# Performance work log

Measured on AMD Instinct MI355X. Metric: run time of the kernel, lower is better.

Reference implementation:

```python
import jax, jax.numpy as jnp
import numpy as np

N = 16384; C = 16; H = 256; W = 704
HEADS = 4; PTS = 4; K = 8; DH = C // HEADS
EPS = 1e-3  # BatchNorm eps from module

def _bn(x, g, b):
    # BatchNorm1d in training mode: batch statistics over N
    mu = x.mean(axis=0)
    var = x.var(axis=0)
    return (x - mu) * jax.lax.rsqrt(var + EPS) * g + b

def setup_inputs():
    key = jax.random.key(0)
    ks = jax.random.split(key, 20)
    def w(i, shape, s=0.25):
        return jax.random.normal(ks[i], shape, jnp.float32) * s
    grid_y = jax.random.randint(ks[0], (N,), 0, H)
    grid_x = jax.random.randint(ks[1], (N,), 0, W)
    return {
        "point_features": jax.random.normal(ks[2], (N, C), jnp.float32),
        "image_feat": jax.random.normal(ks[3], (C, H, W), jnp.float32),
        "image_grid": jnp.stack([grid_y, grid_x], axis=1),
        "Wk": w(4, (C, C)), "bk": w(5, (C,)), "gk": jnp.ones((C,)), "betak": jnp.zeros((C,)),
        "Wfc": w(6, (2, C)), "bfc": w(7, (C,)), "gfc": jnp.ones((C,)), "betafc": jnp.zeros((C,)),
        "Wt": w(8, (C, C)), "bt": w(9, (C,)), "gt": jnp.ones((C,)), "betat": jnp.zeros((C,)),
        "Woff": w(10, (C, HEADS * PTS * 2), 0.02), "boff": w(11, (HEADS * PTS * 2,), 0.5),
        "Wattn": w(12, (C, HEADS * PTS), 0.02), "battn": jnp.zeros((HEADS * PTS,)),
        "Wval": w(13, (C, C)), "bval": w(14, (C,)),
        "Wout": w(15, (C, C)), "bout": w(16, (C,)),
        "Wf": w(17, (2 * C, C)), "bf": w(18, (C,)), "gf": jnp.ones((C,)), "betaf": jnp.zeros((C,)),
    }

def _deform_attn(q, image_feat, grid_f, Woff, boff, Wattn, battn, Wval, bval, Wout, bout):
    # MSDeformAttn with 1 level: learned offsets around projected pixel, bilinear sampling
    n = q.shape[0]
    off = (q @ Woff + boff).reshape(n, HEADS, PTS, 2)
    attn = jax.nn.softmax((q @ Wattn + battn).reshape(n, HEADS, PTS), axis=-1)
    val = (image_feat.reshape(C, H * W).T @ Wval + bval).reshape(H * W, HEADS, DH)
    val_h = val.transpose(1, 0, 2)  # [HEADS, HW, DH]
    loc_y = grid_f[:, 0][:, None, None] + off[..., 0]  # [N, HEADS, PTS]
    loc_x = grid_f[:, 1][:, None, None] + off[..., 1]
    y0 = jnp.floor(loc_y); x0 = jnp.floor(loc_x)
    wy = loc_y - y0; wx = loc_x - x0

    def corner(yi, xi, wgt):
        valid = (yi >= 0) & (yi <= H - 1) & (xi >= 0) & (xi <= W - 1)
        yc = jnp.clip(yi, 0, H - 1).astype(jnp.int32)
        xc = jnp.clip(xi, 0, W - 1).astype(jnp.int32)
        idx = (yc * W + xc).transpose(1, 0, 2)  # [HEADS, N, PTS]
        g = jax.vmap(lambda v, i: v[i])(val_h, idx)  # [HEADS, N, PTS, DH]
        return g * (wgt * valid).transpose(1, 0, 2)[..., None]

    samp = (corner(y0, x0, (1 - wy) * (1 - wx))
            + corner(y0, x0 + 1, (1 - wy) * wx)
            + corner(y0 + 1, x0, wy * (1 - wx))
            + corner(y0 + 1, x0 + 1, wy * wx))  # [HEADS, N, PTS, DH]
    out = (samp * attn.transpose(1, 0, 2)[..., None]).sum(axis=2)  # [HEADS, N, DH]
    out = out.transpose(1, 0, 2).reshape(n, C)
    return out @ Wout + bout

def reference(point_features, image_feat, image_grid, Wk, bk, gk, betak, Wfc, bfc, gfc, betafc, Wt, bt, gt, betat, Woff, boff, Wattn, battn, Wval, bval, Wout, bout, Wf, bf, gf, betaf):
    grid_f = image_grid.astype(jnp.float32)
    # KNN over projected pixel coords (cKDTree.query k=K+1, drop self)
    d2 = ((grid_f[:, None, :] - grid_f[None, :, :]) ** 2).sum(-1)
    _, nidx = jax.lax.top_k(-d2, K + 1)
    nidx = nidx[:, 1:]  # [N, K]

    pts = _bn(point_features @ Wk + bk, gk, betak)  # pts_key_proj
    # normalized relative image-plane positions -> fc
    center = grid_f.mean(axis=0)
    rel = grid_f - center
    mx = jnp.abs(rel).max(axis=0)
    mx = jnp.where(mx == 0, 1.0, mx)
    pos = _bn((rel / mx) @ Wfc + bfc, gfc, betafc)

    # gather image feats at projected pixels + KNN-graph neighbor aggregation
    gathered = image_feat[:, image_grid[:, 0], image_grid[:, 1]].T  # [N, C]
    neigh = gathered[nidx].mean(axis=1)  # [N, C]

    q = pts + pos
    img_pre = _deform_attn(q, image_feat, grid_f, Woff, boff, Wattn, battn, Wval, bval, Wout, bout) + neigh

    pts_pre = _bn(pts @ Wt + bt, gt, betat)  # pts_transform
    fuse = jax.nn.relu(jnp.concatenate([pts_pre, img_pre], axis=-1))  # activate_out
    return jax.nn.relu(_bn(fuse @ Wf + bf, gf, betaf))  # fuse_conv
```

## Files before the change

kernel.cpp:

```cpp
#include <hip/hip_runtime.h>
#include <climits>

#define N_ 16384
#define C_ 16
#define H_ 256
#define W_ 704
#define HW_ (H_*W_)
#define NC_ (N_*C_)
#define EPS_ 1e-3f
#define HDR_ 512

typedef unsigned long long ull;

#define FLIN_  (HDR_ + 8*NC_)
#define VAL_   (HDR_ + 9*NC_)
#define KNNI_  (VAL_ + HW_*16)
#define PARTF_ (KNNI_ + 378256)
#define PS_    (PARTF_ + 16384)
#define GP_    (PS_ + 17408)
#define IMFT_  (GP_ + 640)

#define CAP_ 6144
#define PPB_ 32

#define LOAD16(dst, src) { const float4* _s=(const float4*)(src); float4 _a=_s[0],_b=_s[1],_c=_s[2],_d=_s[3]; \
  dst[0]=_a.x;dst[1]=_a.y;dst[2]=_a.z;dst[3]=_a.w; dst[4]=_b.x;dst[5]=_b.y;dst[6]=_b.z;dst[7]=_b.w; \
  dst[8]=_c.x;dst[9]=_c.y;dst[10]=_c.z;dst[11]=_c.w; dst[12]=_d.x;dst[13]=_d.y;dst[14]=_d.z;dst[15]=_d.w; }

#define STORE16(dst, src) { float4* _d=(float4*)(dst); \
  _d[0]=make_float4(src[0],src[1],src[2],src[3]); _d[1]=make_float4(src[4],src[5],src[6],src[7]); \
  _d[2]=make_float4(src[8],src[9],src[10],src[11]); _d[3]=make_float4(src[12],src[13],src[14],src[15]); }

__global__ __launch_bounds__(256) void k_init(float* ws){
  if (blockIdx.x < 176){
    int4* c = (int4*)(ws + KNNI_);
    c[blockIdx.x*256 + threadIdx.x] = make_int4(0,0,0,0);
  } else if (threadIdx.x == 0){
    int* ih = (int*)ws;
    ih[2]=INT_MAX; ih[3]=INT_MIN; ih[4]=INT_MAX; ih[5]=INT_MIN;
  }
}

__global__ __launch_bounds__(256) void k_statsprep(
    const float* __restrict__ pf, const float* __restrict__ imf,
    const int* __restrict__ grid,
    const float* __restrict__ Wval, const float* __restrict__ bval,
    float* __restrict__ ws)
{
  int t = threadIdx.x;
  if (blockIdx.x < 64){
    __shared__ float sP[4096];
    __shared__ double sDP[20];
    __shared__ int sh[16];
    int i = blockIdx.x*256 + t;
    { const float4* s4=(const float4*)(pf+i*16);
      float4* d4=(float4*)(sP+t*16);
      d4[0]=s4[0]; d4[1]=s4[1]; d4[2]=s4[2]; d4[3]=s4[3]; }
    int2 g = ((const int2*)grid)[i];
    int* counts = (int*)(ws + KNNI_);
    atomicAdd(&counts[g.x*W_ + g.y], 1);
    int mny=g.x,mxy=g.x,mnx=g.y,mxx=g.y;
#pragma unroll
    for (int o=32;o>0;o>>=1){
      mny=min(mny,__shfl_down(mny,o)); mxy=max(mxy,__shfl_down(mxy,o));
      mnx=min(mnx,__shfl_down(mnx,o)); mxx=max(mxx,__shfl_down(mxx,o));
    }
    int wv = t>>6;
    if ((t&63)==0){ sh[wv]=mny; sh[4+wv]=mxy; sh[8+wv]=mnx; sh[12+wv]=mxx; }
    double yy=(double)g.x, xx=(double)g.y;
    double m0=yy,m1=xx,m2=yy*yy,m3=xx*xx,m4=yy*xx;
#pragma unroll
    for (int o=32;o>0;o>>=1){
      m0+=__shfl_down(m0,o); m1+=__shfl_down(m1,o); m2+=__shfl_down(m2,o);
      m3+=__shfl_down(m3,o); m4+=__shfl_down(m4,o);
    }
    if ((t&63)==0){ sDP[wv*5]=m0; sDP[wv*5+1]=m1; sDP[wv*5+2]=m2; sDP[wv*5+3]=m3; sDP[wv*5+4]=m4; }
    __syncthreads();
    if (t==0){
      int* ih=(int*)ws;
      atomicMin(&ih[2],min(min(sh[0],sh[1]),min(sh[2],sh[3])));
      atomicMax(&ih[3],max(max(sh[4],sh[5]),max(sh[6],sh[7])));
      atomicMin(&ih[4],min(min(sh[8],sh[9]),min(sh[10],sh[11])));
      atomicMax(&ih[5],max(max(sh[12],sh[13]),max(sh[14],sh[15])));
      double* GP=(double*)(ws+GP_)+blockIdx.x*5;
#pragma unroll
      for (int k=0;k<5;++k) GP[k]=sDP[k]+sDP[5+k]+sDP[10+k]+sDP[15+k];
    }
    float* PS = ws + PS_ + blockIdx.x*272;
    int a=t&15, b2=t>>4;
    float acc=0.f;
    for (int i2=0;i2<256;++i2) acc += sP[i2*16+a]*sP[i2*16+b2];
    PS[16+t]=acc;
    if (t<16){
      float s=0.f;
      for (int i2=0;i2<256;++i2) s += sP[i2*16+t];
      PS[t]=s;
    }
  } else {
    __shared__ float sW[256], sb[16];
    sW[t]=Wval[t];
    if (t<16) sb[t]=bval[t];
    __syncthreads();
    int pix=(blockIdx.x-64)*256+t;
    float a[16];
#pragma unroll
    for (int ci=0;ci<16;++ci) a[ci]=imf[ci*HW_+pix];
    STORE16(ws+IMFT_+pix*16, a);
    float o[16];
#pragma unroll
    for (int c=0;c<16;++c) o[c]=sb[c];
#pragma unroll
    for (int ci=0;ci<16;++ci){ float v=a[ci];
#pragma unroll
      for (int c=0;c<16;++c) o[c]+=v*sW[ci*16+c];
    }
    STORE16(ws+VAL_+pix*16, o);
  }
}

__global__ __launch_bounds__(256) void k_scanA(float* ws){
  const int* counts = (const int*)(ws + KNNI_);
  int* bsum = (int*)(ws + KNNI_) + 180224 + 180240;
  int t = threadIdx.x;
  int v = counts[blockIdx.x*256 + t];
#pragma unroll
  for (int o=32;o>0;o>>=1) v += __shfl_down(v,o);
  __shared__ int w4[4];
  if ((t&63)==0) w4[t>>6] = v;
  __syncthreads();
  if (t==0) bsum[blockIdx.x] = w4[0]+w4[1]+w4[2]+w4[3];
}

__global__ __launch_bounds__(256) void k_scanB(
    const float* __restrict__ Wk, const float* __restrict__ bk,
    const float* __restrict__ gk, const float* __restrict__ betak,
    const float* __restrict__ Wfc, const float* __restrict__ bfc,
    const float* __restrict__ gfc, const float* __restrict__ betafc,
    const float* __restrict__ Wt, const float* __restrict__ bt,
    const float* __restrict__ gt, const float* __restrict__ betat,
    float* __restrict__ ws)
{
  __shared__ float sS[256], sSum[16];
  __shared__ float skA[16], skC[16];
  __shared__ double sG[5];
  __shared__ float sCtr[4];
  int t = threadIdx.x;
  const float* PS = ws + PS_;
  float acc=0.f, acc2=0.f;
  for (int b=0;b<64;++b){
    acc += PS[b*272 + t];
    if (t<16) acc2 += PS[b*272 + 256 + t];
  }
  if (t<16){ sSum[t]=acc; sS[240+t]=acc2; }
  else sS[t-16]=acc;
  if (t<5){
    const double* GP=(const double*)(ws+GP_);
    double s=0.0;
    for (int b=0;b<64;++b) s += GP[b*5+t];
    sG[t]=s;
  }
  __syncthreads();
  if (t==0){
    const int* ih=(const int*)ws;
    float cy=(float)(sG[0]/(double)N_), cx=(float)(sG[1]/(double)N_);
    float my=fmaxf((float)ih[3]-cy, cy-(float)ih[2]);
    float mx=fmaxf((float)ih[5]-cx, cx-(float)ih[4]);
    if (my==0.f) my=1.f;
    if (mx==0.f) mx=1.f;
    sCtr[0]=cy; sCtr[1]=cx; sCtr[2]=1.f/my; sCtr[3]=1.f/mx;
    ws[264]=cy; ws[265]=cx; ws[266]=sCtr[2]; ws[267]=sCtr[3];
  }
  __syncthreads();
  const float invN = 1.f/(float)N_;
  if (t<16){
    float wc[16];
#pragma unroll
    for (int j=0;j<16;++j) wc[j]=Wk[j*16+t];
    float dotS=0.f;
#pragma unroll
    for (int a2=0;a2<16;++a2) dotS+=sSum[a2]*wc[a2];
    float qd=0.f;
#pragma unroll
    for (int b2=0;b2<16;++b2){
      float inner=0.f;
#pragma unroll
      for (int a2=0;a2<16;++a2) inner+=wc[a2]*sS[b2*16+a2];
      qd+=wc[b2]*inner;
    }
    float bkc=bk[t];
    float mu = dotS*invN + bkc;
    float ex2 = qd*invN + 2.f*bkc*dotS*invN + bkc*bkc;
    float var = ex2 - mu*mu;
    float a = gk[t]/sqrtf(var+EPS_);
    skA[t]=a; skC[t]=betak[t]-mu*a;
    ws[136+t]=a; ws[152+t]=skC[t];
    float cy=sCtr[0], cx=sCtr[1], imy=sCtr[2], imx=sCtr[3];
    float Eyy=((float)(sG[2]/(double)N_) - cy*cy)*imy*imy;
    float Exx=((float)(sG[3]/(double)N_) - cx*cx)*imx*imx;
    float Eyx=((float)(sG[4]/(double)N_) - cy*cx)*imy*imx;
    float W0=Wfc[t], W1=Wfc[16+t];
    float varfc = Eyy*W0*W0 + 2.f*Eyx*W0*W1 + Exx*W1*W1;
    float afc = gfc[t]/sqrtf(varfc+EPS_);
    ws[168+t]=afc; ws[184+t]=betafc[t]-bfc[t]*afc;
  }
  __syncthreads();
  if (t<16){
    float Ac[16];
#pragma unroll
    for (int j=0;j<16;++j){
      float s=0.f;
#pragma unroll
      for (int m=0;m<16;++m) s += Wk[j*16+m]*skA[m]*Wt[m*16+t];
      Ac[j]=s;
    }
    float dc=bt[t];
#pragma unroll
    for (int m=0;m<16;++m) dc += (bk[m]*skA[m]+skC[m])*Wt[m*16+t];
    float dotS=0.f;
#pragma unroll
    for (int a2=0;a2<16;++a2) dotS+=sSum[a2]*Ac[a2];
    float qd=0.f;
#pragma unroll
    for (int b2=0;b2<16;++b2){
      float inner=0.f;
#pragma unroll
      for (int a2=0;a2<16;++a2) inner+=Ac[a2]*sS[b2*16+a2];
      qd+=Ac[b2]*inner;
    }
    float mu = dotS*invN + dc;
    float ex2 = qd*invN + 2.f*dc*dotS*invN + dc*dc;
    float var = ex2 - mu*mu;
    float a = gt[t]/sqrtf(var+EPS_);
    ws[200+t]=a; ws[216+t]=betat[t]-mu*a;
  }
  __syncthreads();
  int* bsum = (int*)(ws + KNNI_) + 180224 + 180240;
  int* boff = bsum + 704;
  __shared__ int sWsum[4];
  __shared__ int sCarry;
  int lane=t&63, wv=t>>6;
  if (t==0) sCarry=0;
  __syncthreads();
  for (int c=0;c<3;++c){
    int idx=c*256+t;
    int v0=(idx<704)?bsum[idx]:0;
    int v=v0;
#pragma unroll
    for (int o=1;o<64;o<<=1){ int xx=__shfl_up(v,o); if (lane>=o) v+=xx; }
    if (lane==63) sWsum[wv]=v;
    __syncthreads();
    int add=sCarry;
    for (int w2=0;w2<wv;++w2) add+=sWsum[w2];
    if (idx<704) boff[idx]=add+v-v0;
    __syncthreads();
    if (t==255) sCarry=add+v;
    __syncthreads();
  }
}

__global__ __launch_bounds__(256) void k_scanC(float* ws){
  int* counts = (int*)(ws + KNNI_);
  int* cellst = counts + 180224;
  const int* boff = counts + 180224 + 180240 + 704;
  __shared__ int sWsum[4];
  int t=threadIdx.x, lane=t&63, wv=t>>6;
  int i=blockIdx.x*256+t;
  int v0=counts[i], v=v0;
#pragma unroll
  for (int o=1;o<64;o<<=1){ int xx=__shfl_up(v,o); if (lane>=o) v+=xx; }
  if (lane==63) sWsum[wv]=v;
  __syncthreads();
  int add=boff[blockIdx.x];
  for (int w2=0;w2<wv;++w2) add+=sWsum[w2];
  int start=add+v-v0;
  cellst[i]=start;
  counts[i]=start;
  if (i==0) cellst[HW_]=N_;
}

__global__ __launch_bounds__(256) void k_scatter(const int* __restrict__ grid, float* __restrict__ ws){
  int i=blockIdx.x*256+threadIdx.x;
  int2 g=((const int2*)grid)[i];
  int* counts=(int*)(ws+KNNI_);
  unsigned* psort=(unsigned*)(counts+180224+180240+704+704);
  int pos=atomicAdd(&counts[g.x*W_+g.y],1);
  psort[pos]=((unsigned)g.x<<24)|((unsigned)g.y<<14)|(unsigned)i;
}

__device__ __forceinline__ void knn_insert(ull* arr, ull key){
  if (key < arr[8]){
    int q=8;
    while (q>0 && arr[q-1]>key){ arr[q]=arr[q-1]; --q; }
    arr[q]=key;
  }
}

__device__ __forceinline__ void scan_rows_global(const int* __restrict__ cellst,
                                                 const unsigned* __restrict__ psort,
                                                 int y, int x, int s,
                                                 int y0, int y1, int x0, int x1, ull* arr){
  for (int yy=y0+s; yy<=y1; yy+=4){
    int rowb=yy*W_;
    int st=cellst[rowb+x0];
    int e =cellst[rowb+x1+1];
    int dy=y-yy, dy2=dy*dy;
    for (int p=st;p<e;++p){
      unsigned u=psort[p];
      int px=(int)((u>>14)&1023);
      int dx=x-px;
      knn_insert(arr, ((ull)(unsigned)(dy2+dx*dx)<<14)|(ull)(u&16383u));
    }
  }
}

__device__ __forceinline__ void scan_rows_band(const unsigned* sBand, const int* sRowBase,
                                               int ya, int y, int x, int s,
                                               int y0, int y1, int x0, int x1, ull* arr){
  for (int yy=y0+s; yy<=y1; yy+=4){
    int j=yy-ya;
    int b=sRowBase[j], e=sRowBase[j+1];
    int lo=b, hi=e;
    while (lo<hi){ int mid=(lo+hi)>>1; int xm=(int)((sBand[mid]>>14)&1023); if (xm<x0) lo=mid+1; else hi=mid; }
    int dy=y-yy, dy2=dy*dy;
    for (int p=lo;p<e;++p){
      unsigned u=sBand[p];
      int px=(int)((u>>14)&1023);
      if (px>x1) break;
      int dx=x-px;
      knn_insert(arr, ((ull)(unsigned)(dy2+dx*dx)<<14)|(ull)(u&16383u));
    }
  }
}

__global__ __launch_bounds__(128) void k_mega(
    const float* __restrict__ pf, const int* __restrict__ grid,
    const float* __restrict__ Wk, const float* __restrict__ bk,
    const float* __restrict__ Wfc, const float* __restrict__ bfc,
    const float* __restrict__ Wt, const float* __restrict__ bt,
    const float* __restrict__ Woff, const float* __restrict__ boff,
    const float* __restrict__ Wattn, const float* __restrict__ battn,
    const float* __restrict__ Wout, const float* __restrict__ bout,
    const float* __restrict__ Wf, const float* __restrict__ bf,
    float* __restrict__ ws)
{
  __shared__ float sWk[256], sWt[256], sWattn[256], sWout[256];
  __shared__ float sWoff[512], sWf[512], sWfc[32];
  __shared__ float sbk[16], sbfc[16], sbt[16], sboff[32], sbattn[16], sbout[16], sbf[16];
  __shared__ float skA[16], skC[16], sfcA[16], sfcC[16], stA[16], stC[16];
  __shared__ float sCtr[4];
  __shared__ unsigned sMe[PPB_];
  __shared__ int sMn, sMx;
  __shared__ unsigned sBand[CAP_];
  __shared__ int sRowBase[80];
  __shared__ float sTl[512], sNei[512], sOf[1024], sAt[512], sSamp[512], sImg[512];
  __shared__ float sPart[64];

  const int* cellst = (const int*)(ws+KNNI_)+180224;
  const unsigned* psort = (const unsigned*)((const int*)(ws+KNNI_)+180224+180240+704+704);
  int tid=threadIdx.x, lane=tid&63;
  for (int j=tid;j<256;j+=128){ sWk[j]=Wk[j]; sWt[j]=Wt[j]; sWattn[j]=Wattn[j]; sWout[j]=Wout[j]; }
  for (int j=tid;j<512;j+=128){ sWoff[j]=Woff[j]; sWf[j]=Wf[j]; }
  if (tid<32){ sWfc[tid]=Wfc[tid]; sboff[tid]=boff[tid]; }
  if (tid<16){
    sbk[tid]=bk[tid]; sbfc[tid]=bfc[tid]; sbt[tid]=bt[tid]; sbattn[tid]=battn[tid];
    sbout[tid]=bout[tid]; sbf[tid]=bf[tid];
    skA[tid]=ws[136+tid]; skC[tid]=ws[152+tid];
    sfcA[tid]=ws[168+tid]; sfcC[tid]=ws[184+tid];
    stA[tid]=ws[200+tid]; stC[tid]=ws[216+tid];
  }
  if (tid<4) sCtr[tid]=ws[264+tid];
  if (tid==0){ sMn=INT_MAX; sMx=-1; }
  if (tid<PPB_) sMe[tid]=psort[blockIdx.x*PPB_+tid];
  __syncthreads();
  if (tid<PPB_){
    int yy=(int)(sMe[tid]>>24);
    atomicMin(&sMn,yy); atomicMax(&sMx,yy);
  }
  __syncthreads();
  int ya=max(sMn-16,0), yb=min(sMx+16,H_-1);
  int nr=yb-ya+1;
  int p0=cellst[ya*W_], p1=cellst[(yb+1)*W_];
  int count=p1-p0;
  bool fb=(count>CAP_)||(nr>78);
  if (tid<PPB_){
    unsigned me=sMe[tid];
    int i=(int)(me&16383u);
    float yf=(float)(me>>24), xf=(float)((me>>14)&1023u);
    float p[16]; LOAD16(p, pf+i*16);
    float ok[16];
#pragma unroll
    for (int c=0;c<16;++c) ok[c]=sbk[c];
#pragma unroll
    for (int j=0;j<16;++j){ float v=p[j];
#pragma unroll
      for (int c=0;c<16;++c) ok[c]+=v*sWk[j*16+c];
    }
    float ry=(yf-sCtr[0])*sCtr[2], rx=(xf-sCtr[1])*sCtr[3];
    float pts[16], q[16];
#pragma unroll
    for (int c=0;c<16;++c){
      pts[c]=ok[c]*skA[c]+skC[c];
      float pos=ry*sWfc[c]+rx*sWfc[16+c]+sbfc[c];
      q[c]=pts[c]+pos*sfcA[c]+sfcC[c];
    }
    float tv[16];
#pragma unroll
    for (int c=0;c<16;++c) tv[c]=sbt[c];
#pragma unroll
    for (int j=0;j<16;++j){ float v=pts[j];
#pragma unroll
      for (int c=0;c<16;++c) tv[c]+=v*sWt[j*16+c];
    }
#pragma unroll
    for (int c=0;c<16;++c) sTl[tid*16+c]=fmaxf(tv[c]*stA[c]+stC[c],0.f);
    float ov[32];
#pragma unroll
    for (int o=0;o<32;++o) ov[o]=sboff[o];
#pragma unroll
    for (int j=0;j<16;++j){ float v=q[j];
#pragma unroll
      for (int o=0;o<32;++o) ov[o]+=v*sWoff[j*32+o];
    }
#pragma unroll
    for (int o=0;o<32;++o) sOf[tid*32+o]=ov[o];
    float l[16];
#pragma unroll
    for (int c=0;c<16;++c) l[c]=sbattn[c];
#pragma unroll
    for (int j=0;j<16;++j){ float v=q[j];
#pragma unroll
      for (int c=0;c<16;++c) l[c]+=v*sWattn[j*16+c];
    }
#pragma unroll
    for (int h=0;h<4;++h){
      float m=fmaxf(fmaxf(l[h*4],l[h*4+1]),fmaxf(l[h*4+2],l[h*4+3]));
      float e0=expf(l[h*4]-m),e1=expf(l[h*4+1]-m),e2=expf(l[h*4+2]-m),e3=expf(l[h*4+3]-m);
      float inv=1.f/(e0+e1+e2+e3);
      sAt[tid*16+h*4]=e0*inv; sAt[tid*16+h*4+1]=e1*inv;
      sAt[tid*16+h*4+2]=e2*inv; sAt[tid*16+h*4+3]=e3*inv;
    }
  } else {
    int tt=tid-PPB_;
    if (!fb){
      for (int j=tt;j<count;j+=96) sBand[j]=psort[p0+j];
      for (int j=tt;j<=nr;j+=96) sRowBase[j]=cellst[(ya+j)*W_]-p0;
    }
  }
  __syncthreads();
  int s=tid&3, pl=tid>>2;
  unsigned meK=sMe[pl];
  int y=(int)(meK>>24), x=(int)((meK>>14)&1023u);
  int r=8;
  { int y0=max(y-8,0),y1=min(y+8,H_-1),x0=max(x-8,0),x1=min(x+8,W_-1);
    if ((y1-y0+1)*(x1-x0+1)<224) r=16; }
  ull arr[9];
#pragma unroll
  for (int q2=0;q2<9;++q2) arr[q2]=~0ull;
  {
    int y0=max(y-r,0),y1=min(y+r,H_-1),x0=max(x-r,0),x1=min(x+r,W_-1);
    if (!fb) scan_rows_band(sBand,sRowBase,ya,y,x,s,y0,y1,x0,x1,arr);
    else     scan_rows_global(cellst,psort,y,x,s,y0,y1,x0,x1,arr);
  }
  ull m[9];
  bool done=false;
  {
    ull k[9];
#pragma unroll
    for (int q2=0;q2<9;++q2) m[q2]=~0ull;
    int base=lane&~3;
    for (int ss=0;ss<4;++ss){
#pragma unroll
      for (int q2=0;q2<9;++q2) k[q2]=__shfl(arr[q2],base+ss);
      for (int q3=0;q3<9;++q3){
        ull kk=k[q3];
        if (kk>=m[8]) break;
        int q=8; while (q>0&&m[q-1]>kk){ m[q]=m[q-1]; --q; } m[q]=kk;
      }
    }
    int y0=max(y-r,0),y1=min(y+r,H_-1),x0=max(x-r,0),x1=min(x+r,W_-1);
    bool covered=(y0==0)&&(y1==H_-1)&&(x0==0)&&(x1==W_-1);
    bool ok2=covered;
    if (!ok2 && m[8]!=~0ull){ int d9=(int)(m[8]>>14); ok2 = d9 < (r+1)*(r+1); }
    done=ok2;
  }
  while (__ballot(!done)){
    if (!done){
      r<<=1;
      int y0=max(y-r,0),y1=min(y+r,H_-1),x0=max(x-r,0),x1=min(x+r,W_-1);
#pragma unroll
      for (int q2=0;q2<9;++q2) arr[q2]=~0ull;
      if (!fb && r<=16) scan_rows_band(sBand,sRowBase,ya,y,x,s,y0,y1,x0,x1,arr);
      else              scan_rows_global(cellst,psort,y,x,s,y0,y1,x0,x1,arr);
    }
    ull k[9];
    bool doIns=!done;
    if (doIns){
#pragma unroll
      for (int q2=0;q2<9;++q2) m[q2]=~0ull;
    }
    int base=lane&~3;
    for (int ss=0;ss<4;++ss){
#pragma unroll
      for (int q2=0;q2<9;++q2) k[q2]=__shfl(arr[q2],base+ss);
      if (doIns){
        for (int q3=0;q3<9;++q3){
          ull kk=k[q3];
          if (kk>=m[8]) break;
          int q=8; while (q>0&&m[q-1]>kk){ m[q]=m[q-1]; --q; } m[q]=kk;
        }
      }
    }
    if (!done){
      int y0=max(y-r,0),y1=min(y+r,H_-1),x0=max(x-r,0),x1=min(x+r,W_-1);
      bool covered=(y0==0)&&(y1==H_-1)&&(x0==0)&&(x1==W_-1);
      bool ok2=covered;
      if (!ok2 && m[8]!=~0ull){ int d9=(int)(m[8]>>14); ok2 = d9 < (r+1)*(r+1); }
      if (ok2) done=true;
    }
  }
  {
    const float* imfT = ws + IMFT_;
    int pixn[8];
#pragma unroll
    for (int nb=0;nb<8;++nb){
      int idx=(int)(m[nb+1]&16383ull);
      int2 g2=((const int2*)grid)[idx];
      pixn[nb]=g2.x*W_+g2.y;
    }
    float4 v[8];
#pragma unroll
    for (int nb=0;nb<8;++nb) v[nb]=*(const float4*)(imfT+pixn[nb]*16+s*4);
    float4 acc=make_float4(0.f,0.f,0.f,0.f);
#pragma unroll
    for (int nb=0;nb<8;++nb){
      acc.x+=v[nb].x; acc.y+=v[nb].y; acc.z+=v[nb].z; acc.w+=v[nb].w;
    }
    ((float4*)sNei)[tid]=make_float4(acc.x*0.125f,acc.y*0.125f,acc.z*0.125f,acc.w*0.125f);
  }
  __syncthreads();
  {
    int p=tid>>2, h=tid&3;
    unsigned meA=sMe[p];
    float yf=(float)(meA>>24), xf=(float)((meA>>14)&1023u);
    const float4* val4=(const float4*)(ws+VAL_);
    int addr[16];
    float wgt[16];
#pragma unroll
    for (int pt=0;pt<4;++pt){
      float a=sAt[p*16+h*4+pt];
      float ly=yf+sOf[p*32+h*8+pt*2], lx=xf+sOf[p*32+h*8+pt*2+1];
      float fy=floorf(ly), fx=floorf(lx);
      float wy=ly-fy, wx=lx-fx;
      int y0=(int)fy, x0=(int)fx;
#pragma unroll
      for (int k2=0;k2<4;++k2){
        int yy=y0+(k2>>1), xx=x0+(k2&1);
        bool valid=((unsigned)yy<(unsigned)H_)&&((unsigned)xx<(unsigned)W_);
        int yc=min(max(yy,0),H_-1), xc=min(max(xx,0),W_-1);
        addr[pt*4+k2]=(yc*W_+xc)*4+h;
        float ww=((k2>>1)?wy:(1.f-wy))*((k2&1)?wx:(1.f-wx));
        wgt[pt*4+k2]=valid?a*ww:0.f;
      }
    }
    float4 acc=make_float4(0.f,0.f,0.f,0.f);
#pragma unroll
    for (int b2=0;b2<2;++b2){
      float4 vv[8];
#pragma unroll
      for (int k2=0;k2<8;++k2) vv[k2]=val4[addr[b2*8+k2]];
#pragma unroll
      for (int k2=0;k2<8;++k2){
        float w2=wgt[b2*8+k2];
        acc.x+=w2*vv[k2].x; acc.y+=w2*vv[k2].y; acc.z+=w2*vv[k2].z; acc.w+=w2*vv[k2].w;
      }
    }
    ((float4*)sSamp)[tid]=acc;
    __syncthreads();
    float img[4];
#pragma unroll
    for (int k2=0;k2<4;++k2){ int cc=h*4+k2; img[k2]=sbout[cc]+sNei[p*16+cc]; }
#pragma unroll
    for (int j=0;j<16;++j){
      float v=sSamp[p*16+j];
#pragma unroll
      for (int k2=0;k2<4;++k2) img[k2]+=v*sWout[j*16+h*4+k2];
    }
    ((float4*)sImg)[tid]=make_float4(img[0],img[1],img[2],img[3]);
    __syncthreads();
    float fl[4];
#pragma unroll
    for (int k2=0;k2<4;++k2) fl[k2]=sbf[h*4+k2];
#pragma unroll
    for (int j=0;j<16;++j){
      float v1=sTl[p*16+j];
      float v2=fmaxf(sImg[p*16+j],0.f);
#pragma unroll
      for (int k2=0;k2<4;++k2){
        fl[k2]+=v1*sWf[j*16+h*4+k2];
        fl[k2]+=v2*sWf[(16+j)*16+h*4+k2];
      }
    }
    int i3=(int)(meA&16383u);
    ((float4*)(ws+FLIN_+i3*16))[h]=make_float4(fl[0],fl[1],fl[2],fl[3]);
    float s0=fl[0],s1=fl[1],s2=fl[2],s3=fl[3];
    float q0=fl[0]*fl[0],q1=fl[1]*fl[1],q2=fl[2]*fl[2],q3=fl[3]*fl[3];
#pragma unroll
    for (int o=32;o>=4;o>>=1){
      s0+=__shfl_down(s0,o); s1+=__shfl_down(s1,o); s2+=__shfl_down(s2,o); s3+=__shfl_down(s3,o);
      q0+=__shfl_down(q0,o); q1+=__shfl_down(q1,o); q2+=__shfl_down(q2,o); q3+=__shfl_down(q3,o);
    }
    int wave=tid>>6, lane2=tid&63;
    if (lane2<4){
      sPart[wave*32+lane2*4+0]=s0; sPart[wave*32+lane2*4+1]=s1;
      sPart[wave*32+lane2*4+2]=s2; sPart[wave*32+lane2*4+3]=s3;
      sPart[wave*32+16+lane2*4+0]=q0; sPart[wave*32+16+lane2*4+1]=q1;
      sPart[wave*32+16+lane2*4+2]=q2; sPart[wave*32+16+lane2*4+3]=q3;
    }
    __syncthreads();
    if (tid<32){
      float v=sPart[tid]+sPart[32+tid];
      (ws+PARTF_)[blockIdx.x*32+tid]=v;
    }
  }
}

__global__ __launch_bounds__(256) void k_outf(const float* __restrict__ gf,
                                              const float* __restrict__ betaf,
                                              const float* __restrict__ ws,
                                              float* __restrict__ out){
  __shared__ float red[256];
  __shared__ float sA[16], sC[16];
  int t=threadIdx.x, slot=t&31, chunk=t>>5;
  const float* part=ws+PARTF_;
  float acc=0.f;
  for (int bb=chunk*64; bb<chunk*64+64; ++bb) acc+=part[bb*32+slot];
  red[t]=acc;
  __syncthreads();
  if (chunk==0){
    float v=red[slot];
#pragma unroll
    for (int k2=1;k2<8;++k2) v+=red[k2*32+slot];
    red[slot]=v;
  }
  __syncthreads();
  if (t<16){
    float mu=red[t]*(1.f/N_);
    float var=red[16+t]*(1.f/N_)-mu*mu;
    float a=gf[t]/sqrtf(var+EPS_);
    sA[t]=a; sC[t]=betaf[t]-mu*a;
  }
  __syncthreads();
  int base=blockIdx.x*4096+t*16;
  float fl[16]; LOAD16(fl, ws+FLIN_+base);
  float o[16];
#pragma unroll
  for (int c=0;c<16;++c) o[c]=fmaxf(fl[c]*sA[c]+sC[c],0.f);
  STORE16(out+base, o);
}

extern "C" void kernel_launch(void* const* d_in, const int* in_sizes, int n_in,
                              void* d_out, int out_size, void* d_ws, size_t ws_size,
                              hipStream_t stream)
{
  const float* pf    = (const float*)d_in[0];
  const float* imf   = (const float*)d_in[1];
  const int*   gridp = (const int*)d_in[2];
  const float* Wk   =(const float*)d_in[3],  *bk   =(const float*)d_in[4];
  const float* gk   =(const float*)d_in[5],  *betak=(const float*)d_in[6];
  const float* Wfc  =(const float*)d_in[7],  *bfc  =(const float*)d_in[8];
  const float* gfc  =(const float*)d_in[9],  *betafc=(const float*)d_in[10];
  const float* Wt   =(const float*)d_in[11], *bt   =(const float*)d_in[12];
  const float* gt   =(const float*)d_in[13], *betat=(const float*)d_in[14];
  const float* Woff =(const float*)d_in[15], *boff =(const float*)d_in[16];
  const float* Wattn=(const float*)d_in[17], *battn=(const float*)d_in[18];
  const float* Wval =(const float*)d_in[19], *bval =(const float*)d_in[20];
  const float* Wout =(const float*)d_in[21], *bout =(const float*)d_in[22];
  const float* Wf   =(const float*)d_in[23], *bf   =(const float*)d_in[24];
  const float* gf   =(const float*)d_in[25], *betaf=(const float*)d_in[26];
  float* ws  = (float*)d_ws;
  float* out = (float*)d_out;

  hipLaunchKernelGGL(k_init,      dim3(177),     dim3(256), 0, stream, ws);
  hipLaunchKernelGGL(k_statsprep, dim3(768),     dim3(256), 0, stream, pf, imf, gridp, Wval, bval, ws);
  hipLaunchKernelGGL(k_scanA,     dim3(704),     dim3(256), 0, stream, ws);
  hipLaunchKernelGGL(k_scanB,     dim3(1),       dim3(256), 0, stream,
                     Wk, bk, gk, betak, Wfc, bfc, gfc, betafc, Wt, bt, gt, betat, ws);
  hipLaunchKernelGGL(k_scanC,     dim3(704),     dim3(256), 0, stream, ws);
  hipLaunchKernelGGL(k_scatter,   dim3(N_/256),  dim3(256), 0, stream, gridp, ws);
  hipLaunchKernelGGL(k_mega,      dim3(N_/PPB_), dim3(128), 0, stream,
                     pf, gridp, Wk, bk, Wfc, bfc, Wt, bt, Woff, boff, Wattn, battn,
                     Wout, bout, Wf, bf, ws);
  hipLaunchKernelGGL(k_outf,      dim3(64),      dim3(256), 0, stream, gf, betaf, ws, out);
}
```

Measured before the change: 234.8 us.

## Prefetch deformable samples before KNN, pack coords in keys, shrink shared memory

Moves the bilinear-sample address computation and the 16 value gathers for deformable attention ahead of the KNN search, so those global loads are in flight while the KNN scan runs. KNN keys now store the distance in the high 32 bits plus index and pixel coordinates, which removes the extra grid lookup per neighbour. sSamp and sImg now reuse the sBand buffer, and the band capacity shrinks, cutting LDS use so more blocks can be resident. The costs are 16 float4 values held in registers across the KNN phase, which can raise register pressure, and a global-read fallback more often when a band does not fit the smaller buffer. The key ordering also changes, so ties in distance now break by index first and then by coordinates.

Result: no change. 236.0 us (+0.5%).

```diff
diff --git a/kernel.cpp b/kernel.cpp
--- a/kernel.cpp
+++ b/kernel.cpp
@@ -20,7 +20,7 @@
 #define GP_    (PS_ + 17408)
 #define IMFT_  (GP_ + 640)
 
-#define CAP_ 6144
+#define CAP_ 3584
 #define PPB_ 32
 
 #define LOAD16(dst, src) { const float4* _s=(const float4*)(src); float4 _a=_s[0],_b=_s[1],_c=_s[2],_d=_s[3]; \
@@ -287,6 +287,11 @@
   psort[pos]=((unsigned)g.x<<24)|((unsigned)g.y<<14)|(unsigned)i;
 }
 
+__device__ __forceinline__ ull make_key(int d2, unsigned u){
+  return ((ull)(unsigned)d2<<32) | ((ull)(u&16383u)<<18) |
+         ((ull)(u>>24)<<10) | (ull)((u>>14)&1023u);
+}
+
 __device__ __forceinline__ void knn_insert(ull* arr, ull key){
   if (key < arr[8]){
     int q=8;
@@ -308,7 +313,7 @@
       unsigned u=psort[p];
       int px=(int)((u>>14)&1023);
       int dx=x-px;
-      knn_insert(arr, ((ull)(unsigned)(dy2+dx*dx)<<14)|(ull)(u&16383u));
+      knn_insert(arr, make_key(dy2+dx*dx, u));
     }
   }
 }
@@ -327,13 +332,13 @@
       int px=(int)((u>>14)&1023);
       if (px>x1) break;
       int dx=x-px;
-      knn_insert(arr, ((ull)(unsigned)(dy2+dx*dx)<<14)|(ull)(u&16383u));
+      knn_insert(arr, make_key(dy2+dx*dx, u));
     }
   }
 }
 
 __global__ __launch_bounds__(128) void k_mega(
-    const float* __restrict__ pf, const int* __restrict__ grid,
+    const float* __restrict__ pf,
     const float* __restrict__ Wk, const float* __restrict__ bk,
     const float* __restrict__ Wfc, const float* __restrict__ bfc,
     const float* __restrict__ Wt, const float* __restrict__ bt,
@@ -352,8 +357,10 @@
   __shared__ int sMn, sMx;
   __shared__ unsigned sBand[CAP_];
   __shared__ int sRowBase[80];
-  __shared__ float sTl[512], sNei[512], sOf[1024], sAt[512], sSamp[512], sImg[512];
+  __shared__ float sTl[512], sNei[512], sOf[1024], sAt[512];
   __shared__ float sPart[64];
+  float* sSamp = (float*)sBand;
+  float* sImg  = ((float*)sBand) + 512;
 
   const int* cellst = (const int*)(ws+KNNI_)+180224;
   const unsigned* psort = (const unsigned*)((const int*)(ws+KNNI_)+180224+180240+704+704);
@@ -448,6 +455,33 @@
   }
   __syncthreads();
   int s=tid&3, pl=tid>>2;
+  float4 pv[16];
+  float pwgt[16];
+  {
+    unsigned meA=sMe[pl];
+    float yf=(float)(meA>>24), xf=(float)((meA>>14)&1023u);
+    const float4* val4=(const float4*)(ws+VAL_);
+    int addr[16];
+#pragma unroll
+    for (int pt=0;pt<4;++pt){
+      float a=sAt[pl*16+s*4+pt];
+      float ly=yf+sOf[pl*32+s*8+pt*2], lx=xf+sOf[pl*32+s*8+pt*2+1];
+      float fy=floorf(ly), fx=floorf(lx);
+      float wy=ly-fy, wx=lx-fx;
+      int y0=(int)fy, x0=(int)fx;
+#pragma unroll
+      for (int k2=0;k2<4;++k2){
+        int yy=y0+(k2>>1), xx=x0+(k2&1);
+        bool valid=((unsigned)yy<(unsigned)H_)&&((unsigned)xx<(unsigned)W_);
+        int yc=min(max(yy,0),H_-1), xc=min(max(xx,0),W_-1);
+        addr[pt*4+k2]=(yc*W_+xc)*4+s;
+        float ww=((k2>>1)?wy:(1.f-wy))*((k2&1)?wx:(1.f-wx));
+        pwgt[pt*4+k2]=valid?a*ww:0.f;
+      }
+    }
+#pragma unroll
+    for (int k2=0;k2<16;++k2) pv[k2]=val4[addr[k2]];
+  }
   unsigned meK=sMe[pl];
   int y=(int)(meK>>24), x=(int)((meK>>14)&1023u);
   int r=8;
@@ -480,7 +514,7 @@
     int y0=max(y-r,0),y1=min(y+r,H_-1),x0=max(x-r,0),x1=min(x+r,W_-1);
     bool covered=(y0==0)&&(y1==H_-1)&&(x0==0)&&(x1==W_-1);
     bool ok2=covered;
-    if (!ok2 && m[8]!=~0ull){ int d9=(int)(m[8]>>14); ok2 = d9 < (r+1)*(r+1); }
+    if (!ok2 && m[8]!=~0ull){ int d9=(int)(m[8]>>32); ok2 = d9 < (r+1)*(r+1); }
     done=ok2;
   }
   while (__ballot(!done)){
@@ -514,7 +548,7 @@
       int y0=max(y-r,0),y1=min(y+r,H_-1),x0=max(x-r,0),x1=min(x+r,W_-1);
       bool covered=(y0==0)&&(y1==H_-1)&&(x0==0)&&(x1==W_-1);
       bool ok2=covered;
-      if (!ok2 && m[8]!=~0ull){ int d9=(int)(m[8]>>14); ok2 = d9 < (r+1)*(r+1); }
+      if (!ok2 && m[8]!=~0ull){ int d9=(int)(m[8]>>32); ok2 = d9 < (r+1)*(r+1); }
       if (ok2) done=true;
     }
   }
@@ -523,9 +557,8 @@
     int pixn[8];
 #pragma unroll
     for (int nb=0;nb<8;++nb){
-      int idx=(int)(m[nb+1]&16383ull);
-      int2 g2=((const int2*)grid)[idx];
-      pixn[nb]=g2.x*W_+g2.y;
+      ull mk=m[nb+1];
+      pixn[nb]=(int)((mk>>10)&255ull)*W_ + (int)(mk&1023ull);
     }
     float4 v[8];
 #pragma unroll
@@ -539,40 +572,12 @@
   }
   __syncthreads();
   {
-    int p=tid>>2, h=tid&3;
-    unsigned meA=sMe[p];
-    float yf=(float)(meA>>24), xf=(float)((meA>>14)&1023u);
-    const float4* val4=(const float4*)(ws+VAL_);
-    int addr[16];
-    float wgt[16];
-#pragma unroll
-    for (int pt=0;pt<4;++pt){
-      float a=sAt[p*16+h*4+pt];
-      float ly=yf+sOf[p*32+h*8+pt*2], lx=xf+sOf[p*32+h*8+pt*2+1];
-      float fy=floorf(ly), fx=floorf(lx);
-      float wy=ly-fy, wx=lx-fx;
-      int y0=(int)fy, x0=(int)fx;
-#pragma unroll
-      for (int k2=0;k2<4;++k2){
-        int yy=y0+(k2>>1), xx=x0+(k2&1);
-        bool valid=((unsigned)yy<(unsigned)H_)&&((unsigned)xx<(unsigned)W_);
-        int yc=min(max(yy,0),H_-1), xc=min(max(xx,0),W_-1);
-        addr[pt*4+k2]=(yc*W_+xc)*4+h;
-        float ww=((k2>>1)?wy:(1.f-wy))*((k2&1)?wx:(1.f-wx));
-        wgt[pt*4+k2]=valid?a*ww:0.f;
-      }
-    }
+    int p=pl, h=s;
     float4 acc=make_float4(0.f,0.f,0.f,0.f);
 #pragma unroll
-    for (int b2=0;b2<2;++b2){
-      float4 vv[8];
-#pragma unroll
-      for (int k2=0;k2<8;++k2) vv[k2]=val4[addr[b2*8+k2]];
-#pragma unroll
-      for (int k2=0;k2<8;++k2){
-        float w2=wgt[b2*8+k2];
-        acc.x+=w2*vv[k2].x; acc.y+=w2*vv[k2].y; acc.z+=w2*vv[k2].z; acc.w+=w2*vv[k2].w;
-      }
+    for (int k2=0;k2<16;++k2){
+      float w2=pwgt[k2];
+      acc.x+=w2*pv[k2].x; acc.y+=w2*pv[k2].y; acc.z+=w2*pv[k2].z; acc.w+=w2*pv[k2].w;
     }
     ((float4*)sSamp)[tid]=acc;
     __syncthreads();
@@ -600,6 +605,7 @@
         fl[k2]+=v2*sWf[(16+j)*16+h*4+k2];
       }
     }
+    unsigned meA=sMe[p];
     int i3=(int)(meA&16383u);
     ((float4*)(ws+FLIN_+i3*16))[h]=make_float4(fl[0],fl[1],fl[2],fl[3]);
     float s0=fl[0],s1=fl[1],s2=fl[2],s3=fl[3];
@@ -688,7 +694,7 @@
   hipLaunchKernelGGL(k_scanC,     dim3(704),     dim3(256), 0, stream, ws);
   hipLaunchKernelGGL(k_scatter,   dim3(N_/256),  dim3(256), 0, stream, gridp, ws);
   hipLaunchKernelGGL(k_mega,      dim3(N_/PPB_), dim3(128), 0, stream,
-                     pf, gridp, Wk, bk, Wfc, bfc, Wt, bt, Woff, boff, Wattn, battn,
+                     pf, Wk, bk, Wfc, bfc, Wt, bt, Woff, boff, Wattn, battn,
                      Wout, bout, Wf, bf, ws);
   hipLaunchKernelGGL(k_outf,      dim3(64),      dim3(256), 0, stream, gf, betaf, ws, out);
 }
```
